# Optimization experiments

Hardware: AMD Instinct MI355X
Metric: run time of the kernel (lower is better)

The kernel has to match this reference:

```python
import jax, jax.numpy as jnp
import numpy as np

B, D, H, T, F = 2, 256, 8, 128, 64
C = H * F          # channels = 512
TE = 512           # time_embed_dim


def setup_inputs() -> dict:
    key = jax.random.key(0)
    ks = jax.random.split(key, 9)
    pd = jax.random.randint(ks[2], (B, T, T), 0, 2 * T - 1, dtype=jnp.int32) - (T - 1)
    s = 0.02
    return {
        "qk": jax.random.normal(ks[0], (B, D, H, T, F), jnp.float32),
        "temb": jax.random.normal(ks[1], (B, T, TE), jnp.float32),
        "pairwise_distances": pd,
        "w_dist": jax.random.normal(ks[3], (3, C), jnp.float32) * s,
        "b_dist": jax.random.normal(ks[4], (C,), jnp.float32) * s,
        "w_time": jax.random.normal(ks[5], (TE, C), jnp.float32) * s,
        "b_time": jax.random.normal(ks[6], (C,), jnp.float32) * s,
        "w_out": jax.random.normal(ks[7], (C, C), jnp.float32) * s,
        "b_out": jax.random.normal(ks[8], (C,), jnp.float32) * s,
    }


def _rpe_net(temb, pd, w_dist, b_dist, w_time, b_time, w_out, b_out):
    d = pd.astype(jnp.float32)
    # (B, T, S, 3): log(1+d+), log(1+d-), indicator(d==0)
    dist_embs = jnp.stack(
        [jnp.log1p(jnp.maximum(d, 0.0)),
         jnp.log1p(jnp.maximum(-d, 0.0)),
         (pd == 0).astype(jnp.float32)],
        axis=-1,
    )
    emb = (temb @ w_time + b_time)[:, :, None, :] + dist_embs @ w_dist + b_dist  # (B,T,S,C)
    R = jax.nn.silu(emb) @ w_out + b_out  # (B,T,S,C)
    return R.reshape(*pd.shape, H, F)     # (B,T,S,H,F)


def reference(qk, temb, pairwise_distances, w_dist, b_dist, w_time, b_time, w_out, b_out):
    R = _rpe_net(temb, pairwise_distances, w_dist, b_dist, w_time, b_time, w_out, b_out)
    # forward_qk: contract head_dim f for every (t, s) pair
    return jnp.einsum('bdhtf,btshf->bdhts', qk, R)
```

## Files before the change

kernel.cpp:

```cpp
#include <hip/hip_runtime.h>
#include <hip/hip_bf16.h>

#define B_  2
#define D_  256
#define H_  8
#define T_  128
#define S_  128
#define F_  64
#define C_  512
#define TE_ 512

typedef _Float16 f16x8 __attribute__((ext_vector_type(8)));
typedef _Float16 f16x4 __attribute__((ext_vector_type(4)));
typedef float    f32x4 __attribute__((ext_vector_type(4)));

#define AS1 __attribute__((address_space(1)))
#define AS3 __attribute__((address_space(3)))

__global__ __launch_bounds__(128) void k_time_proj(
    const float* __restrict__ temb, const float* __restrict__ w_time,
    const float* __restrict__ b_time, const float* __restrict__ b_dist,
    float* __restrict__ tp)
{
    int row = blockIdx.x;
    int tid = threadIdx.x;
    __shared__ float te[TE_];
    for (int i = tid; i < TE_; i += 128)
        te[i] = temb[(size_t)row * TE_ + i];
    __syncthreads();
    int c0 = tid * 4;
    float4 b0 = *(const float4*)&b_time[c0];
    float4 b1 = *(const float4*)&b_dist[c0];
    float ax0 = 0.f, ay0 = 0.f, az0 = 0.f, aw0 = 0.f;
    float ax1 = 0.f, ay1 = 0.f, az1 = 0.f, aw1 = 0.f;
#pragma unroll 4
    for (int e = 0; e < TE_; e += 2) {
        float s0 = te[e], s1 = te[e + 1];
        float4 w0 = *(const float4*)&w_time[(size_t)e * C_ + c0];
        float4 w1 = *(const float4*)&w_time[(size_t)(e + 1) * C_ + c0];
        ax0 += s0 * w0.x; ay0 += s0 * w0.y; az0 += s0 * w0.z; aw0 += s0 * w0.w;
        ax1 += s1 * w1.x; ay1 += s1 * w1.y; az1 += s1 * w1.z; aw1 += s1 * w1.w;
    }
    float4 r;
    r.x = b0.x + b1.x + ax0 + ax1;
    r.y = b0.y + b1.y + ay0 + ay1;
    r.z = b0.z + b1.z + az0 + az1;
    r.w = b0.w + b1.w + aw0 + aw1;
    *(float4*)&tp[(size_t)row * C_ + c0] = r;
}

__global__ __launch_bounds__(128) void k_embed_silu(
    const float* __restrict__ tp, const int* __restrict__ pd,
    const float* __restrict__ w_dist, _Float16* __restrict__ A)
{
    int row = blockIdx.x;
    int bt  = row >> 7;
    int d   = pd[row];
    float f0 = log1pf(fmaxf((float)d, 0.f));
    float f1 = log1pf(fmaxf((float)(-d), 0.f));
    float f2 = (d == 0) ? 1.f : 0.f;
    int c0 = threadIdx.x * 4;
    float4 t4 = *(const float4*)&tp[(size_t)bt * C_ + c0];
    float4 w0 = *(const float4*)&w_dist[c0];
    float4 w1 = *(const float4*)&w_dist[C_ + c0];
    float4 w2 = *(const float4*)&w_dist[2 * C_ + c0];
    float e0 = t4.x + f0 * w0.x + f1 * w1.x + f2 * w2.x;
    float e1 = t4.y + f0 * w0.y + f1 * w1.y + f2 * w2.y;
    float e2 = t4.z + f0 * w0.z + f1 * w1.z + f2 * w2.z;
    float e3 = t4.w + f0 * w0.w + f1 * w1.w + f2 * w2.w;
    f16x4 v;
    v[0] = (_Float16)(e0 / (1.f + expf(-e0)));
    v[1] = (_Float16)(e1 / (1.f + expf(-e1)));
    v[2] = (_Float16)(e2 / (1.f + expf(-e2)));
    v[3] = (_Float16)(e3 / (1.f + expf(-e3)));
    *(f16x4*)&A[(size_t)row * C_ + c0] = v;
}

__global__ __launch_bounds__(512) void k_wt(
    const float* __restrict__ w_out, _Float16* __restrict__ Wt)
{
    int n = blockIdx.x;
    int k = threadIdx.x;
    Wt[(size_t)n * C_ + k] = (_Float16)w_out[(size_t)k * C_ + n];
}

__global__ __launch_bounds__(512, 4) void k_fused(
    const float* __restrict__ qk, const _Float16* __restrict__ A,
    const _Float16* __restrict__ Wt, const float* __restrict__ b_out,
    float* __restrict__ out)
{
    __shared__ alignas(16) char smem[65536];
    char* asb = smem;
    char* wtb = smem + 16384;
    char* rsb = smem;

    int bt = blockIdx.x >> 1;
    int hg = blockIdx.x & 1;
    int b  = bt >> 7, t = bt & 127;
    int tid  = threadIdx.x;
    int wave = tid >> 6, lane = tid & 63;
    int mrow = lane & 15, kq = (lane >> 4) * 8;
    int swz  = (mrow & 7) << 4;
    int grow = lane >> 3;
    int gcol = ((lane & 7) ^ grow) * 8;

    int wm1 = (wave & 1) * 64;
    int wn1 = (wave >> 1) * 64;
    const size_t arow0 = (size_t)bt * 128;
    f32x4 acc[4][4] = {};
    for (int k0 = 0; k0 < 512; k0 += 64) {
#pragma unroll
        for (int q = 0; q < 2; ++q) {
            int ch = wave * 2 + q;
            __builtin_amdgcn_global_load_lds(
                (const AS1 void*)(const void*)&A[(arow0 + ch * 8 + grow) * 512 + k0 + gcol],
                (AS3 void*)(void*)(asb + ch * 1024), 16, 0, 0);
        }
#pragma unroll
        for (int q = 0; q < 4; ++q) {
            int ch = wave * 4 + q;
            __builtin_amdgcn_global_load_lds(
                (const AS1 void*)(const void*)&Wt[(size_t)(hg * 256 + ch * 8 + grow) * 512 + k0 + gcol],
                (AS3 void*)(void*)(wtb + ch * 1024), 16, 0, 0);
        }
        __syncthreads();
#pragma unroll
        for (int ks = 0; ks < 64; ks += 32) {
            f16x8 af[4], wtf[4];
#pragma unroll
            for (int i = 0; i < 4; ++i) {
                int row = wm1 + i * 16 + mrow;
                af[i] = *(const f16x8*)(asb + (((row << 7) + ((ks + kq) << 1)) ^ swz));
            }
#pragma unroll
            for (int j = 0; j < 4; ++j) {
                int row = wn1 + j * 16 + mrow;
                wtf[j] = *(const f16x8*)(wtb + (((row << 7) + ((ks + kq) << 1)) ^ swz));
            }
#pragma unroll
            for (int j = 0; j < 4; ++j)
#pragma unroll
                for (int i = 0; i < 4; ++i)
                    acc[j][i] = __builtin_amdgcn_mfma_f32_16x16x32_f16(wtf[j], af[i], acc[j][i], 0, 0, 0);
        }
        __syncthreads();
    }
    {
        int cg = (lane >> 4) * 4;
#pragma unroll
        for (int j = 0; j < 4; ++j) {
            int c = wn1 + j * 16 + cg;
            float4 bo = *(const float4*)&b_out[hg * 256 + c];
#pragma unroll
            for (int i = 0; i < 4; ++i) {
                int s = wm1 + i * 16 + mrow;
                f16x4 hv;
                hv[0] = (_Float16)(acc[j][i][0] + bo.x);
                hv[1] = (_Float16)(acc[j][i][1] + bo.y);
                hv[2] = (_Float16)(acc[j][i][2] + bo.z);
                hv[3] = (_Float16)(acc[j][i][3] + bo.w);
                *(f16x4*)(rsb + (((s << 9) + (c << 1)) ^ swz)) = hv;
            }
        }
    }
    __syncthreads();

    int wm2 = (wave >> 1) * 64;
    int wn2 = (wave & 1) * 64;
    const size_t qstr = (size_t)(H_ * T_ * F_);
    const size_t ostr = (size_t)(H_ * T_ * S_);
    int dcol = lane & 15, sb = (lane >> 4) * 4;
    for (int hp = 0; hp < 4; ++hp) {
        int h = hg * 4 + hp;
        const size_t qbase = (size_t)b * (D_ * H_ * T_ * F_) + (size_t)h * (T_ * F_)
                           + (size_t)t * F_;
        f32x4 acc2[4][4] = {};
#pragma unroll
        for (int ks = 0; ks < 64; ks += 32) {
            f16x8 rf[4], qf[4];
#pragma unroll
            for (int j = 0; j < 4; ++j) {
                int s = wn2 + j * 16 + mrow;
                rf[j] = *(const f16x8*)(rsb + (((s << 9) + ((hp * 64 + ks + kq) << 1)) ^ swz));
            }
#pragma unroll
            for (int i = 0; i < 4; ++i) {
                const float* qp = &qk[qbase + (size_t)(wm2 + i * 16 + mrow) * qstr + ks + kq];
                float4 u = *(const float4*)qp;
                float4 v = *(const float4*)(qp + 4);
                f16x8 a;
                a[0] = (_Float16)u.x; a[1] = (_Float16)u.y;
                a[2] = (_Float16)u.z; a[3] = (_Float16)u.w;
                a[4] = (_Float16)v.x; a[5] = (_Float16)v.y;
                a[6] = (_Float16)v.z; a[7] = (_Float16)v.w;
                qf[i] = a;
            }
#pragma unroll
            for (int j = 0; j < 4; ++j)
#pragma unroll
                for (int i = 0; i < 4; ++i)
                    acc2[j][i] = __builtin_amdgcn_mfma_f32_16x16x32_f16(rf[j], qf[i], acc2[j][i], 0, 0, 0);
        }
        const size_t obase = (size_t)b * (D_ * H_ * T_ * S_) + (size_t)h * (T_ * S_)
                           + (size_t)t * S_;
#pragma unroll
        for (int i = 0; i < 4; ++i) {
            size_t orow = obase + (size_t)(wm2 + i * 16 + dcol) * ostr;
#pragma unroll
            for (int j = 0; j < 4; ++j)
                *(f32x4*)&out[orow + wn2 + j * 16 + sb] = acc2[j][i];
        }
    }
}

extern "C" void kernel_launch(void* const* d_in, const int* in_sizes, int n_in,
                              void* d_out, int out_size, void* d_ws, size_t ws_size,
                              hipStream_t stream) {
    (void)in_sizes; (void)n_in; (void)out_size; (void)ws_size;
    const float* qk     = (const float*)d_in[0];
    const float* temb   = (const float*)d_in[1];
    const int*   pd     = (const int*)d_in[2];
    const float* w_dist = (const float*)d_in[3];
    const float* b_dist = (const float*)d_in[4];
    const float* w_time = (const float*)d_in[5];
    const float* b_time = (const float*)d_in[6];
    const float* w_out  = (const float*)d_in[7];
    const float* b_out  = (const float*)d_in[8];
    float* out = (float*)d_out;

    char* ws = (char*)d_ws;
    float*     tp = (float*)ws;
    _Float16*  Wt = (_Float16*)(ws + 512 * 1024);
    _Float16*  A  = (_Float16*)(ws + 1024 * 1024);

    k_time_proj<<<dim3(B_ * T_), dim3(128), 0, stream>>>(temb, w_time, b_time, b_dist, tp);
    k_wt<<<dim3(C_), dim3(C_), 0, stream>>>(w_out, Wt);
    k_embed_silu<<<dim3(B_ * T_ * S_), dim3(128), 0, stream>>>(tp, pd, w_dist, A);
    k_fused<<<dim3(B_ * T_ * 2), dim3(512), 0, stream>>>(qk, A, Wt, b_out, out);
}
```

Before: 500.4 us.

## Fuse distance embedding and SiLU into the GEMM kernel's A-tile staging

Removes the separate k_embed_silu kernel and the fp16 activation buffer A. Each k_fused block now stages the time projection row and w_dist in LDS and computes the embedding and SiLU for its A tile in registers. It then writes the result straight into swizzled shared memory instead of loading it from global memory. This drops a large intermediate write and read plus one launch. In exchange, the exp-heavy SiLU is recomputed twice (once per head-group block), and the main loop carries extra ALU work and LDS use.

After: 478.5 us. -4.4%, faster.

```diff
diff --git a/kernel.cpp b/kernel.cpp
--- a/kernel.cpp
+++ b/kernel.cpp
@@ -49,33 +49,6 @@
     *(float4*)&tp[(size_t)row * C_ + c0] = r;
 }
 
-__global__ __launch_bounds__(128) void k_embed_silu(
-    const float* __restrict__ tp, const int* __restrict__ pd,
-    const float* __restrict__ w_dist, _Float16* __restrict__ A)
-{
-    int row = blockIdx.x;
-    int bt  = row >> 7;
-    int d   = pd[row];
-    float f0 = log1pf(fmaxf((float)d, 0.f));
-    float f1 = log1pf(fmaxf((float)(-d), 0.f));
-    float f2 = (d == 0) ? 1.f : 0.f;
-    int c0 = threadIdx.x * 4;
-    float4 t4 = *(const float4*)&tp[(size_t)bt * C_ + c0];
-    float4 w0 = *(const float4*)&w_dist[c0];
-    float4 w1 = *(const float4*)&w_dist[C_ + c0];
-    float4 w2 = *(const float4*)&w_dist[2 * C_ + c0];
-    float e0 = t4.x + f0 * w0.x + f1 * w1.x + f2 * w2.x;
-    float e1 = t4.y + f0 * w0.y + f1 * w1.y + f2 * w2.y;
-    float e2 = t4.z + f0 * w0.z + f1 * w1.z + f2 * w2.z;
-    float e3 = t4.w + f0 * w0.w + f1 * w1.w + f2 * w2.w;
-    f16x4 v;
-    v[0] = (_Float16)(e0 / (1.f + expf(-e0)));
-    v[1] = (_Float16)(e1 / (1.f + expf(-e1)));
-    v[2] = (_Float16)(e2 / (1.f + expf(-e2)));
-    v[3] = (_Float16)(e3 / (1.f + expf(-e3)));
-    *(f16x4*)&A[(size_t)row * C_ + c0] = v;
-}
-
 __global__ __launch_bounds__(512) void k_wt(
     const float* __restrict__ w_out, _Float16* __restrict__ Wt)
 {
@@ -85,14 +58,16 @@
 }
 
 __global__ __launch_bounds__(512, 4) void k_fused(
-    const float* __restrict__ qk, const _Float16* __restrict__ A,
+    const float* __restrict__ qk, const float* __restrict__ tp,
+    const int* __restrict__ pd, const float* __restrict__ w_dist,
     const _Float16* __restrict__ Wt, const float* __restrict__ b_out,
     float* __restrict__ out)
 {
     __shared__ alignas(16) char smem[65536];
-    char* asb = smem;
-    char* wtb = smem + 16384;
-    char* rsb = smem;
+    char*  asb = smem;
+    char*  wtb = smem + 16384;
+    float* tpw = (float*)(smem + 49152);
+    char*  rsb = smem;
 
     int bt = blockIdx.x >> 1;
     int hg = blockIdx.x & 1;
@@ -104,18 +79,29 @@
     int grow = lane >> 3;
     int gcol = ((lane & 7) ^ grow) * 8;
 
+    tpw[tid]        = tp[(size_t)bt * 512 + tid];
+    tpw[512 + tid]  = w_dist[tid];
+    tpw[1024 + tid] = w_dist[512 + tid];
+    tpw[1536 + tid] = w_dist[1024 + tid];
+
+    int as_s  = tid >> 2;
+    int as_cb = (tid & 3) * 16;
+    int as_swz = (as_s & 7) << 4;
+    int dpd = pd[bt * 128 + as_s];
+    float f0 = log1pf(fmaxf((float)dpd, 0.f));
+    float f1 = log1pf(fmaxf((float)(-dpd), 0.f));
+    float f2 = (dpd == 0) ? 1.f : 0.f;
+    __syncthreads();
+
+    const float* tpL = tpw;
+    const float* w0L = tpw + 512;
+    const float* w1L = tpw + 1024;
+    const float* w2L = tpw + 1536;
+
     int wm1 = (wave & 1) * 64;
     int wn1 = (wave >> 1) * 64;
-    const size_t arow0 = (size_t)bt * 128;
     f32x4 acc[4][4] = {};
     for (int k0 = 0; k0 < 512; k0 += 64) {
-#pragma unroll
-        for (int q = 0; q < 2; ++q) {
-            int ch = wave * 2 + q;
-            __builtin_amdgcn_global_load_lds(
-                (const AS1 void*)(const void*)&A[(arow0 + ch * 8 + grow) * 512 + k0 + gcol],
-                (AS3 void*)(void*)(asb + ch * 1024), 16, 0, 0);
-        }
 #pragma unroll
         for (int q = 0; q < 4; ++q) {
             int ch = wave * 4 + q;
@@ -123,6 +109,29 @@
                 (const AS1 void*)(const void*)&Wt[(size_t)(hg * 256 + ch * 8 + grow) * 512 + k0 + gcol],
                 (AS3 void*)(void*)(wtb + ch * 1024), 16, 0, 0);
         }
+        float ev[16];
+#pragma unroll
+        for (int u4 = 0; u4 < 4; ++u4) {
+            int k = k0 + as_cb + u4 * 4;
+            float4 tv = *(const float4*)&tpL[k];
+            float4 a0 = *(const float4*)&w0L[k];
+            float4 a1 = *(const float4*)&w1L[k];
+            float4 a2 = *(const float4*)&w2L[k];
+            ev[u4 * 4 + 0] = tv.x + f0 * a0.x + f1 * a1.x + f2 * a2.x;
+            ev[u4 * 4 + 1] = tv.y + f0 * a0.y + f1 * a1.y + f2 * a2.y;
+            ev[u4 * 4 + 2] = tv.z + f0 * a0.z + f1 * a1.z + f2 * a2.z;
+            ev[u4 * 4 + 3] = tv.w + f0 * a0.w + f1 * a1.w + f2 * a2.w;
+        }
+        f16x8 h0, h1;
+#pragma unroll
+        for (int u = 0; u < 8; ++u) {
+            float e0 = ev[u], e1 = ev[8 + u];
+            h0[u] = (_Float16)(e0 / (1.f + expf(-e0)));
+            h1[u] = (_Float16)(e1 / (1.f + expf(-e1)));
+        }
+        int cb2 = as_cb * 2;
+        *(f16x8*)(asb + (((as_s << 7) + cb2)      ^ as_swz)) = h0;
+        *(f16x8*)(asb + (((as_s << 7) + cb2 + 16) ^ as_swz)) = h1;
         __syncthreads();
 #pragma unroll
         for (int ks = 0; ks < 64; ks += 32) {
@@ -231,10 +240,8 @@
     char* ws = (char*)d_ws;
     float*     tp = (float*)ws;
     _Float16*  Wt = (_Float16*)(ws + 512 * 1024);
-    _Float16*  A  = (_Float16*)(ws + 1024 * 1024);
 
     k_time_proj<<<dim3(B_ * T_), dim3(128), 0, stream>>>(temb, w_time, b_time, b_dist, tp);
     k_wt<<<dim3(C_), dim3(C_), 0, stream>>>(w_out, Wt);
-    k_embed_silu<<<dim3(B_ * T_ * S_), dim3(128), 0, stream>>>(tp, pd, w_dist, A);
-    k_fused<<<dim3(B_ * T_ * 2), dim3(512), 0, stream>>>(qk, A, Wt, b_out, out);
-}
+    k_fused<<<dim3(B_ * T_ * 2), dim3(512), 0, stream>>>(qk, tp, pd, w_dist, Wt, b_out, out);
+}
```
